# Kernel optimization log

Measured on AMD Instinct MI355X. Metric: run time of the kernel, lower is better.

Reference implementation:

```python
import jax, jax.numpy as jnp
import numpy as np

N_STMT, N_FUNC = 100000, 50000
T, V, C, H, L, E = 16, 50000, 128, 8, 2, 200000
D = C // H  # per-head dim = 16
N_NODES = (N_STMT, N_FUNC)
# (src_type, dst_type) for the 3 relations: stmt->stmt, stmt->func, func->stmt
EDGE_TYPES = ((0, 0), (0, 1), (1, 0))


def _segment_softmax(logits, seg, num_segments):
    # logits: [E, H], seg: [E] destination node ids
    m = jax.ops.segment_max(logits, seg, num_segments)
    m = jnp.where(jnp.isfinite(m), m, 0.0)
    e = jnp.exp(logits - m[seg])
    s = jax.ops.segment_sum(e, seg, num_segments)
    return e / (s[seg] + 1e-16)


def setup_inputs() -> dict:
    key = jax.random.key(0)
    ks = jax.random.split(key, 24)
    nrm = lambda k, sh, s=0.1: jax.random.normal(k, sh, dtype=jnp.float32) * s
    ri = lambda k, sh, hi: jax.random.randint(k, sh, 0, hi, dtype=jnp.int32)
    return {
        "tok_stmt": ri(ks[0], (N_STMT, T), V),
        "tok_func": ri(ks[1], (N_FUNC, T), V),
        "e0_src": ri(ks[2], (E,), N_STMT), "e0_dst": ri(ks[3], (E,), N_STMT),
        "e1_src": ri(ks[4], (E,), N_STMT), "e1_dst": ri(ks[5], (E,), N_FUNC),
        "e2_src": ri(ks[6], (E,), N_FUNC), "e2_dst": ri(ks[7], (E,), N_STMT),
        "emb": nrm(ks[8], (V, C), 0.5),
        "lin_w": nrm(ks[9], (2, C, C)), "lin_b": jnp.zeros((2, C), jnp.float32),
        "kw": nrm(ks[10], (L, 2, C, C)), "kb": jnp.zeros((L, 2, C), jnp.float32),
        "qw": nrm(ks[11], (L, 2, C, C)), "qb": jnp.zeros((L, 2, C), jnp.float32),
        "vw": nrm(ks[12], (L, 2, C, C)), "vb": jnp.zeros((L, 2, C), jnp.float32),
        "aw": nrm(ks[13], (L, 2, C, C)), "ab": jnp.zeros((L, 2, C), jnp.float32),
        "skip": jnp.ones((L, 2), jnp.float32),
        "a_rel": nrm(ks[14], (L, 3, H, D, D), 0.25),
        "m_rel": nrm(ks[15], (L, 3, H, D, D), 0.25),
        "p_rel": jnp.ones((L, 3, H), jnp.float32),
    }


def _hgt_forward(tok_stmt, tok_func, edges, emb, lin_w, lin_b,
                 kw, kb, qw, qb, vw, vb, aw, ab, skip, a_rel, m_rel, p_rel):
    # STEncoder (embedding + mean pool) + relu, then per-type linear + relu
    xs = []
    for t, tok in enumerate((tok_stmt, tok_func)):
        e = jax.nn.relu(jnp.mean(emb[tok], axis=1))          # [N_t, C]
        xs.append(jax.nn.relu(e @ lin_w[t] + lin_b[t]))      # [N_t, C]

    scale = 1.0 / jnp.sqrt(jnp.float32(D))
    for l in range(L):
        k = [(x @ kw[l, t] + kb[l, t]).reshape(-1, H, D) for t, x in enumerate(xs)]
        q = [(x @ qw[l, t] + qb[l, t]).reshape(-1, H, D) for t, x in enumerate(xs)]
        v = [(x @ vw[l, t] + vb[l, t]).reshape(-1, H, D) for t, x in enumerate(xs)]
        agg = [jnp.zeros((N_NODES[t], H, D), xs[t].dtype) for t in range(2)]
        for r, (st, dt) in enumerate(EDGE_TYPES):
            src, dst = edges[r]
            k_r = jnp.einsum('nhd,hde->nhe', k[st], a_rel[l, r])
            v_r = jnp.einsum('nhd,hde->nhe', v[st], m_rel[l, r])
            logits = jnp.sum(q[dt][dst] * k_r[src], axis=-1) * p_rel[l, r] * scale  # [E,H]
            alpha = _segment_softmax(logits, dst, N_NODES[dt])
            msg = v_r[src] * alpha[..., None]                 # [E,H,D]
            agg[dt] = agg[dt] + jax.ops.segment_sum(msg, dst, N_NODES[dt])
        new_xs = []
        for t in range(2):
            o = jax.nn.gelu(agg[t].reshape(N_NODES[t], C))
            o = o @ aw[l, t] + ab[l, t]
            g = jax.nn.sigmoid(skip[l, t])
            new_xs.append(g * o + (1.0 - g) * xs[t])
        xs = new_xs
    return jnp.concatenate(xs, axis=0)  # [N_STMT + N_FUNC, C]


def reference(tok_stmt, tok_func, e0_src, e0_dst, e1_src, e1_dst, e2_src, e2_dst,
              emb, lin_w, lin_b, kw, kb, qw, qb, vw, vb, aw, ab, skip,
              a_rel, m_rel, p_rel):
    edges = ((e0_src, e0_dst), (e1_src, e1_dst), (e2_src, e2_dst))
    return _hgt_forward(tok_stmt, tok_func, edges, emb, lin_w, lin_b,
                        kw, kb, qw, qb, vw, vb, aw, ab, skip, a_rel, m_rel, p_rel)
```

## Files before the change

### kernel.cpp

```cpp
#include <hip/hip_runtime.h>
#include <hip/hip_bf16.h>


typedef __hip_bfloat16 bf16;
typedef __attribute__((ext_vector_type(8))) short short8;
typedef __attribute__((ext_vector_type(4))) short s4v;
typedef __attribute__((ext_vector_type(4))) float floatx4;

#define N_STMT 100000
#define N_FUNC 50000
#define N_TOT  150000
#define EDGES  200000
#define CCH 128
#define RPB2 96
#define GS2 1042
#define GF2 521

__device__ __forceinline__ float b2f(bf16 x){ return __bfloat162float(x); }
__device__ __forceinline__ float bs2f(short s){
  union { short s; bf16 h; } u; u.s = s; return __bfloat162float(u.h);
}
__device__ __forceinline__ short f2bs(float x){
  union { bf16 h; short s; } u; u.h = __float2bfloat16(x); return u.s;
}
__device__ __forceinline__ float blo(unsigned u){ return __uint_as_float(u << 16); }
__device__ __forceinline__ float bhi(unsigned u){ return __uint_as_float(u & 0xffff0000u); }
__device__ __forceinline__ float gelu_f(float x){
  float z = 1.5957691216057308f * (x + 0.044715f * x * x * x);
  float t = __expf(z);
  return x - x / (t + 1.f);
}

__global__ __launch_bounds__(256) void emb2bf(
    const float* __restrict__ emb, bf16* __restrict__ ebf)
{
  long i = ((long)blockIdx.x * 256 + threadIdx.x) * 8;
  float4 f0 = *(const float4*)(emb + i);
  float4 f1 = *(const float4*)(emb + i + 4);
  short8 o;
  o[0]=f2bs(f0.x); o[1]=f2bs(f0.y); o[2]=f2bs(f0.z); o[3]=f2bs(f0.w);
  o[4]=f2bs(f1.x); o[5]=f2bs(f1.y); o[6]=f2bs(f1.z); o[7]=f2bs(f1.w);
  *(short8*)(ebf + i) = o;
}

__global__ __launch_bounds__(256) void pool_embed(
    const int* __restrict__ tok_s, const int* __restrict__ tok_f,
    const bf16* __restrict__ ebf, bf16* __restrict__ E_out)
{
  int n = blockIdx.x * 4 + (threadIdx.x >> 6);
  int lane = threadIdx.x & 63, g = lane >> 4, c16 = lane & 15;
  const int* tok = (n < N_STMT) ? (tok_s + n * 16) : (tok_f + (n - N_STMT) * 16);
  float acc[8] = {0.f,0.f,0.f,0.f,0.f,0.f,0.f,0.f};
#pragma unroll
  for (int j = 0; j < 4; j++) {
    int v = tok[g * 4 + j];
    short8 row = *(const short8*)(ebf + (long)v * CCH + c16 * 8);
#pragma unroll
    for (int q = 0; q < 8; q++) acc[q] += bs2f(row[q]);
  }
#pragma unroll
  for (int q = 0; q < 8; q++) {
    acc[q] += __shfl_xor(acc[q], 16);
    acc[q] += __shfl_xor(acc[q], 32);
  }
  if (g == 0) {
    short8 o;
#pragma unroll
    for (int q = 0; q < 8; q++) o[q] = f2bs(fmaxf(acc[q] * (1.f/16.f), 0.f));
    *(short8*)(E_out + (long)n * CCH + c16 * 8) = o;
  }
}

__global__ __launch_bounds__(256) void transp_w(
    const float* __restrict__ lin_w, const float* __restrict__ qw,
    const float* __restrict__ aw, bf16* __restrict__ out)
{
  int mat = blockIdx.y;
  const float* src = (mat < 2) ? lin_w + mat * 16384
                   : (mat < 6) ? qw + (mat - 2) * 16384
                               : aw + (mat - 6) * 16384;
  bf16* dst = out + mat * 16384;
  int idx = blockIdx.x * 256 + threadIdx.x;
  int n = idx >> 7, k = idx & 127;
  dst[idx] = __float2bfloat16(src[k * 128 + n]);
}

__global__ __launch_bounds__(256) void make_wr_all(
    const float* __restrict__ kw, const float* __restrict__ kb,
    const float* __restrict__ vw, const float* __restrict__ vb,
    const float* __restrict__ a_rel, const float* __restrict__ m_rel,
    bf16* __restrict__ WRT, float* __restrict__ Bf)
{
  int y = blockIdx.y;
  bool isV = y >= 6;
  int z = isV ? y - 6 : y;
  int l = z / 3, r = z % 3, st = (r == 2) ? 1 : 0;
  const float* W   = (isV ? vw : kw) + (l * 2 + st) * 16384;
  const float* b   = (isV ? vb : kb) + (l * 2 + st) * 128;
  const float* rel = (isV ? m_rel : a_rel) + z * 2048;
  bf16* Wrt = WRT + y * 16384;
  float* br = Bf + y * 128;

  int idx = blockIdx.x * 256 + threadIdx.x;
  if (idx < 128 * 128) {
    int c = idx >> 7, o = idx & 127;
    int h = o >> 4, e = o & 15;
    float acc = 0.f;
#pragma unroll
    for (int d = 0; d < 16; d++)
      acc += W[c * 128 + h * 16 + d] * rel[h * 256 + d * 16 + e];
    Wrt[o * 128 + c] = __float2bfloat16(acc);
  }
  if (idx < 128) {
    int h = idx >> 4, e = idx & 15;
    float acc = 0.f;
#pragma unroll
    for (int d = 0; d < 16; d++)
      acc += b[h * 16 + d] * rel[h * 256 + d * 16 + e];
    br[idx] = acc;
  }
}

template <bool RELU, bool BLEND, bool OUT_BF16>
__global__ __launch_bounds__(256) void gemm_2t_reg(
    const bf16* __restrict__ Ab, const bf16* __restrict__ Wt0,
    const bf16* __restrict__ Wt1, const float* __restrict__ bias0,
    const float* __restrict__ bias1, const bf16* __restrict__ oldx,
    void* __restrict__ dstv, const float* __restrict__ skip2)
{
  const int wave = threadIdx.x >> 6, lane = threadIdx.x & 63;
  const int lane15 = lane & 15, quad = lane >> 4;
  const int jc0 = wave * 2;
  const int bid = blockIdx.x;
  const int type = (bid >= GS2);
  const long base = type ? (long)N_STMT * CCH : 0;
  const int Nrows = type ? N_FUNC : N_STMT;
  long row = (long)(type ? bid - GS2 : bid) * RPB2;
  long rowEnd = row + RPB2; if (rowEnd > Nrows) rowEnd = Nrows;
  const bf16* Wt = type ? Wt1 : Wt0;
  const float* bias = type ? bias1 : bias0;

  short8 w[2][4];
#pragma unroll
  for (int jj = 0; jj < 2; jj++)
#pragma unroll
    for (int kq = 0; kq < 4; kq++)
      w[jj][kq] = *(const short8*)(
          Wt + ((jc0 + jj) * 16 + lane15) * CCH + kq * 32 + quad * 8);
  float4 bb[2];
#pragma unroll
  for (int jj = 0; jj < 2; jj++)
    bb[jj] = *(const float4*)(bias + (jc0 + jj) * 16 + quad * 4);

  float g = 1.f, gi = 0.f;
  if (BLEND) {
    float sk = skip2[type];
    g = 1.f / (1.f + expf(-sk));
    gi = 1.f - g;
  }

  short8 a[4];
  {
    long r = row + lane15; if (r >= Nrows) r = Nrows - 1;
#pragma unroll
    for (int kq = 0; kq < 4; kq++)
      a[kq] = *(const short8*)(Ab + base + r * CCH + kq * 32 + quad * 8);
  }

  for (; row < rowEnd; row += 16) {
    short8 an[4];
    {
      long nrow = (row + 16 < rowEnd) ? row + 16 : row;
      long r = nrow + lane15; if (r >= Nrows) r = Nrows - 1;
#pragma unroll
      for (int kq = 0; kq < 4; kq++)
        an[kq] = *(const short8*)(Ab + base + r * CCH + kq * 32 + quad * 8);
    }

    floatx4 acc[2];
#pragma unroll
    for (int jj = 0; jj < 2; jj++) {
      acc[jj][0] = bb[jj].x; acc[jj][1] = bb[jj].y;
      acc[jj][2] = bb[jj].z; acc[jj][3] = bb[jj].w;
    }
#pragma unroll
    for (int kq = 0; kq < 4; kq++)
#pragma unroll
      for (int jj = 0; jj < 2; jj++)
        acc[jj] = __builtin_amdgcn_mfma_f32_16x16x32_bf16(
            w[jj][kq], a[kq], acc[jj], 0, 0, 0);

    long r = row + lane15;
    if (r < Nrows) {
#pragma unroll
      for (int jj = 0; jj < 2; jj++) {
        int c0 = (jc0 + jj) * 16 + quad * 4;
        long idx = base + r * CCH + c0;
        float v[4];
#pragma unroll
        for (int q = 0; q < 4; q++) v[q] = acc[jj][q];
        if (RELU) {
#pragma unroll
          for (int q = 0; q < 4; q++) v[q] = fmaxf(v[q], 0.f);
        }
        if (BLEND) {
          s4v ov = *(const s4v*)(oldx + idx);
#pragma unroll
          for (int q = 0; q < 4; q++) v[q] = g * v[q] + gi * bs2f(ov[q]);
        }
        if (OUT_BF16) {
          s4v o;
#pragma unroll
          for (int q = 0; q < 4; q++) o[q] = f2bs(v[q]);
          *(s4v*)((bf16*)dstv + idx) = o;
        } else {
          float4 o = make_float4(v[0], v[1], v[2], v[3]);
          *(float4*)((float*)dstv + idx) = o;
        }
      }
    }
#pragma unroll
    for (int kq = 0; kq < 4; kq++) a[kq] = an[kq];
  }
}

template <int NM, bool HASQ>
__global__ __launch_bounds__(256, (NM == 2 ? 4 : 3)) void gemm_qkv_reg(
    const bf16* __restrict__ Ab,
    const bf16* __restrict__ W0, const float* __restrict__ B0,
    const bf16* __restrict__ W1, const float* __restrict__ B1,
    const bf16* __restrict__ W2, const float* __restrict__ B2,
    bf16* __restrict__ Q, bf16* __restrict__ KV, int N, int rpb)
{
  const int wave = threadIdx.x >> 6, lane = threadIdx.x & 63;
  const int lane15 = lane & 15, quad = lane >> 4;
  const int jc0 = wave * 2;
  constexpr int KIDX = HASQ ? 1 : 0;
  constexpr int VIDX = KIDX + 1;

  long row = (long)blockIdx.x * rpb;
  if (row >= N) return;
  long rowEnd = row + rpb; if (rowEnd > N) rowEnd = N;

  const bf16* Wm[3]  = {W0, W1, W2};
  const float* Bm[3] = {B0, B1, B2};

  short8 w[NM][2][4];
#pragma unroll
  for (int m = 0; m < NM; m++)
#pragma unroll
    for (int jj = 0; jj < 2; jj++)
#pragma unroll
      for (int kq = 0; kq < 4; kq++)
        w[m][jj][kq] = *(const short8*)(
            Wm[m] + ((jc0 + jj) * 16 + lane15) * CCH + kq * 32 + quad * 8);

  for (; row < rowEnd; row += 16) {
    long r = row + lane15;
    long rc = (r < N) ? r : (N - 1);
    short8 a[4];
#pragma unroll
    for (int kq = 0; kq < 4; kq++)
      a[kq] = *(const short8*)(Ab + rc * CCH + kq * 32 + quad * 8);

    floatx4 acc[NM][2];
#pragma unroll
    for (int m = 0; m < NM; m++)
#pragma unroll
      for (int jj = 0; jj < 2; jj++) {
        float4 bb = *(const float4*)(Bm[m] + (jc0 + jj) * 16 + quad * 4);
        acc[m][jj][0] = bb.x; acc[m][jj][1] = bb.y;
        acc[m][jj][2] = bb.z; acc[m][jj][3] = bb.w;
      }

#pragma unroll
    for (int kq = 0; kq < 4; kq++)
#pragma unroll
      for (int m = 0; m < NM; m++)
#pragma unroll
        for (int jj = 0; jj < 2; jj++)
          acc[m][jj] = __builtin_amdgcn_mfma_f32_16x16x32_bf16(
              w[m][jj][kq], a[kq], acc[m][jj], 0, 0, 0);

    if (r < N) {
#pragma unroll
      for (int jj = 0; jj < 2; jj++) {
        int c0 = (jc0 + jj) * 16 + quad * 4;
        if constexpr (HASQ) {
          s4v qo;
          qo[0] = f2bs(acc[0][jj][0]);
          qo[1] = f2bs(acc[0][jj][1]);
          qo[2] = f2bs(acc[0][jj][2]);
          qo[3] = f2bs(acc[0][jj][3]);
          *(s4v*)(Q + r * CCH + c0) = qo;
        }
        short8 kv;
        kv[0] = f2bs(acc[KIDX][jj][0]);
        kv[1] = f2bs(acc[KIDX][jj][1]);
        kv[2] = f2bs(acc[VIDX][jj][0]);
        kv[3] = f2bs(acc[VIDX][jj][1]);
        kv[4] = f2bs(acc[KIDX][jj][2]);
        kv[5] = f2bs(acc[KIDX][jj][3]);
        kv[6] = f2bs(acc[VIDX][jj][2]);
        kv[7] = f2bs(acc[VIDX][jj][3]);
        *(short8*)(KV + r * 256 + 2 * c0) = kv;
      }
    }
  }
}

__global__ __launch_bounds__(256) void csr_count(
    const int* __restrict__ dst, int* __restrict__ deg, int* __restrict__ pos)
{
  int e = blockIdx.x * 256 + threadIdx.x;
  if (e < EDGES) pos[e] = atomicAdd(&deg[dst[e]], 1);
}
__global__ __launch_bounds__(256) void csr_alloc(
    const int* __restrict__ deg, int* __restrict__ rowstart,
    int* __restrict__ total, int Ndst)
{
  int n = blockIdx.x * 256 + threadIdx.x;
  if (n < Ndst) rowstart[n] = atomicAdd(total, deg[n]);
}
__global__ __launch_bounds__(256) void csr_fill(
    const int* __restrict__ dst, const int* __restrict__ src,
    const int* __restrict__ rowstart, const int* __restrict__ pos,
    int* __restrict__ srcs)
{
  int e = blockIdx.x * 256 + threadIdx.x;
  if (e < EDGES) srcs[rowstart[dst[e]] + pos[e]] = src[e];
}

__device__ __forceinline__ void relmsg_grp(
    int rs, int g, const int* __restrict__ srcs,
    const bf16* __restrict__ KV, float psc,
    const float* __restrict__ q, int lane, float* __restrict__ out)
{
  int p = lane & 15;
  int gbase = lane & 48;
  float den = 0.f;
  float a[8] = {0.f,0.f,0.f,0.f,0.f,0.f,0.f,0.f};
  for (int j0 = 0; j0 < g; j0 += 16) {
    int rem = g - j0; if (rem > 16) rem = 16;
    int sl = srcs[rs + j0 + (p < rem ? p : rem - 1)];
    for (int j = 0; j < rem; j++) {
      int s = __shfl(sl, gbase + j);
      const bf16* rowp = KV + (long)s * 256 + 16 * p;
      uint4 u0 = *(const uint4*)(rowp);
      uint4 u1 = *(const uint4*)(rowp + 8);
      float prod = q[0]*blo(u0.x) + q[1]*bhi(u0.x)
                 + q[2]*blo(u0.z) + q[3]*bhi(u0.z)
                 + q[4]*blo(u1.x) + q[5]*bhi(u1.x)
                 + q[6]*blo(u1.z) + q[7]*bhi(u1.z);
      prod += __shfl_xor(prod, 1);
      float ev = __expf(prod * psc);
      den += ev;
      a[0] += ev * blo(u0.y); a[1] += ev * bhi(u0.y);
      a[2] += ev * blo(u0.w); a[3] += ev * bhi(u0.w);
      a[4] += ev * blo(u1.y); a[5] += ev * bhi(u1.y);
      a[6] += ev * blo(u1.w); a[7] += ev * bhi(u1.w);
    }
  }
  float inv = 1.f / (den + 1e-16f);
#pragma unroll
  for (int i = 0; i < 8; i++) out[i] = a[i] * inv;
}

__global__ __launch_bounds__(256) void agg_all(
    const int* __restrict__ rs0, const int* __restrict__ dg0, const int* __restrict__ srcs0,
    const int* __restrict__ rs1, const int* __restrict__ dg1, const int* __restrict__ srcs1,
    const int* __restrict__ rs2, const int* __restrict__ dg2, const int* __restrict__ srcs2,
    const bf16* __restrict__ KV0, const bf16* __restrict__ KV1,
    const bf16* __restrict__ KV2, const float* __restrict__ pl,
    const bf16* __restrict__ Qb, bf16* __restrict__ AGGb)
{
  int n = blockIdx.x * 16 + (threadIdx.x >> 4);
  if (n >= N_TOT) return;
  int lane = threadIdx.x & 63;
  int p = lane & 15, h = p >> 1;
  uint4 qv = *(const uint4*)(Qb + (long)n * CCH + 8 * p);
  float q[8];
  q[0] = blo(qv.x); q[1] = bhi(qv.x); q[2] = blo(qv.y); q[3] = bhi(qv.y);
  q[4] = blo(qv.z); q[5] = bhi(qv.z); q[6] = blo(qv.w); q[7] = bhi(qv.w);
  float m[8];
  if (n < N_STMT) {
    float m0[8], m2[8];
    relmsg_grp(rs0[n], dg0[n], srcs0, KV0, pl[h] * 0.25f, q, lane, m0);
    relmsg_grp(rs2[n], dg2[n], srcs2, KV2, pl[16 + h] * 0.25f, q, lane, m2);
#pragma unroll
    for (int i = 0; i < 8; i++) m[i] = m0[i] + m2[i];
  } else {
    int nf = n - N_STMT;
    relmsg_grp(rs1[nf], dg1[nf], srcs1, KV1, pl[8 + h] * 0.25f, q, lane, m);
  }
  short8 o;
#pragma unroll
  for (int i = 0; i < 8; i++) o[i] = f2bs(gelu_f(m[i]));
  *(short8*)(AGGb + (long)n * CCH + 8 * p) = o;
}

__global__ __launch_bounds__(256) void zero_out_k(float* __restrict__ out)
{
  long i = ((long)blockIdx.x * 256 + threadIdx.x) * 4;
  *(float4*)(out + i) = make_float4(0.f, 0.f, 0.f, 0.f);
}

extern "C" void kernel_launch(void* const* d_in, const int* in_sizes, int n_in,
                              void* d_out, int out_size, void* d_ws, size_t ws_size,
                              hipStream_t stream)
{
  const int* tok_s = (const int*)d_in[0];
  const int* tok_f = (const int*)d_in[1];
  const int* esrc[3] = {(const int*)d_in[2], (const int*)d_in[4], (const int*)d_in[6]};
  const int* edst[3] = {(const int*)d_in[3], (const int*)d_in[5], (const int*)d_in[7]};
  const float* emb   = (const float*)d_in[8];
  const float* lin_w = (const float*)d_in[9];
  const float* lin_b = (const float*)d_in[10];
  const float* kw = (const float*)d_in[11];
  const float* kb = (const float*)d_in[12];
  const float* qw = (const float*)d_in[13];
  const float* qb = (const float*)d_in[14];
  const float* vw = (const float*)d_in[15];
  const float* vb = (const float*)d_in[16];
  const float* aw = (const float*)d_in[17];
  const float* ab = (const float*)d_in[18];
  const float* skip  = (const float*)d_in[19];
  const float* a_rel = (const float*)d_in[20];
  const float* m_rel = (const float*)d_in[21];
  const float* p_rel = (const float*)d_in[22];

  float* Bf   = (float*)d_ws;
  bf16*  Xb   = (bf16*)(Bf + 1536);
  bf16*  AGGb = Xb  + 19200000L;
  bf16*  KV0  = AGGb + 19200000L;
  bf16*  KV1  = KV0 + 25600000L;
  bf16*  KV2  = KV1 + 25600000L;
  bf16*  WT   = KV2 + 12800000L;
  bf16*  WRT  = WT  + 163840L;
  int*   ip   = (int*)(WRT + 196608L);
  int* deg[3]      = {ip, ip + 100000, ip + 150000};
  int* total       = ip + 250000;
  int* rowstart[3] = {ip + 250004, ip + 350004, ip + 400004};
  int* srcs[3]     = {ip + 500004, ip + 700004, ip + 900004};
  int* pos         = ip + 1100004;
  bf16* EBF   = KV0;
  bf16*  Qb   = (bf16*)d_out;
  float* OUTF = (float*)d_out;

  const size_t NEED = (size_t)1536 * 4 + (size_t)102760448 * 2
                    + (size_t)1300004 * 4;
  if (ws_size < NEED) {
    zero_out_k<<<19200000 / 4 / 256, 256, 0, stream>>>(OUTF);
    return;
  }

  const int  Ntype[2] = {N_STMT, N_FUNC};
  const int  edt[3] = {0, 1, 0};
  const int  EB = (EDGES + 255) / 256;

  hipMemsetAsync(ip, 0, (size_t)250004 * 4, stream);
  for (int r = 0; r < 3; r++) {
    int Nd = Ntype[edt[r]];
    csr_count<<<EB, 256, 0, stream>>>(edst[r], deg[r], pos);
    csr_alloc<<<(Nd + 255) / 256, 256, 0, stream>>>(deg[r], rowstart[r], total + r, Nd);
    csr_fill<<<EB, 256, 0, stream>>>(edst[r], esrc[r], rowstart[r], pos, srcs[r]);
  }

  emb2bf<<<3125, 256, 0, stream>>>(emb, EBF);
  transp_w<<<dim3(64, 10), 256, 0, stream>>>(lin_w, qw, aw, WT);
  make_wr_all<<<dim3(64, 12), 256, 0, stream>>>(kw, kb, vw, vb, a_rel, m_rel, WRT, Bf);

  pool_embed<<<N_TOT / 4, 256, 0, stream>>>(tok_s, tok_f, EBF, AGGb);
  gemm_2t_reg<true, false, true><<<GS2 + GF2, 256, 0, stream>>>(
      AGGb, WT, WT + 16384, lin_b, lin_b + 128, nullptr, Xb, nullptr);

  const int GA = (N_STMT + 127) / 128;
  const int GB = (N_STMT + 95) / 96;
  const int GF = (N_FUNC + 127) / 128;

  for (int l = 0; l < 2; l++) {
    int z0 = l * 3 + 0, z1 = l * 3 + 1, z2 = l * 3 + 2;
    gemm_qkv_reg<3, true><<<GA, 256, 0, stream>>>(
        Xb,
        WT + (2 + l * 2) * 16384, qb + (l * 2) * 128,
        WRT + z0 * 16384, Bf + z0 * 128,
        WRT + (6 + z0) * 16384, Bf + (6 + z0) * 128,
        Qb, KV0, N_STMT, 128);
    gemm_qkv_reg<2, false><<<GB, 256, 0, stream>>>(
        Xb,
        WRT + z1 * 16384, Bf + z1 * 128,
        WRT + (6 + z1) * 16384, Bf + (6 + z1) * 128,
        nullptr, nullptr,
        nullptr, KV1, N_STMT, 96);
    gemm_qkv_reg<3, true><<<GF, 256, 0, stream>>>(
        Xb + (long)N_STMT * CCH,
        WT + (2 + l * 2 + 1) * 16384, qb + (l * 2 + 1) * 128,
        WRT + z2 * 16384, Bf + z2 * 128,
        WRT + (6 + z2) * 16384, Bf + (6 + z2) * 128,
        Qb + (long)N_STMT * CCH, KV2, N_FUNC, 128);
    agg_all<<<(N_TOT + 15) / 16, 256, 0, stream>>>(
        rowstart[0], deg[0], srcs[0], rowstart[1], deg[1], srcs[1],
        rowstart[2], deg[2], srcs[2], KV0, KV1, KV2,
        p_rel + l * 24, Qb, AGGb);
    if (l == 0)
      gemm_2t_reg<false, true, true><<<GS2 + GF2, 256, 0, stream>>>(
          AGGb, WT + 6 * 16384, WT + 7 * 16384, ab, ab + 128,
          Xb, Xb, skip);
    else
      gemm_2t_reg<false, true, false><<<GS2 + GF2, 256, 0, stream>>>(
          AGGb, WT + 8 * 16384, WT + 9 * 16384, ab + 256, ab + 384,
          Xb, OUTF, skip + 2);
  }
}
```

Before: 719.5 us.

## Fuse embedding mean-pool with per-type input linear layer via MFMA

Replaces the separate pooling kernel and the following GEMM with a single kernel. Each block pools 64 rows into LDS as bf16 A-fragments and immediately applies the per-type 128x128 linear, bias and ReLU with MFMA. This removes the write and re-read of the intermediate pooled matrix and one launch. In exchange, weights are reloaded per 64-row block and each thread holds more gather accumulators, which may lower occupancy.

```diff
diff --git a/kernel.cpp b/kernel.cpp
--- a/kernel.cpp
+++ b/kernel.cpp
@@ -15,6 +15,8 @@
 #define RPB2 96
 #define GS2 1042
 #define GF2 521
+#define GSP 1563
+#define GFP 782
 
 __device__ __forceinline__ float b2f(bf16 x){ return __bfloat162float(x); }
 __device__ __forceinline__ float bs2f(short s){
@@ -43,31 +45,103 @@
   *(short8*)(ebf + i) = o;
 }
 
-__global__ __launch_bounds__(256) void pool_embed(
+__global__ __launch_bounds__(256, 3) void pool_lin(
     const int* __restrict__ tok_s, const int* __restrict__ tok_f,
-    const bf16* __restrict__ ebf, bf16* __restrict__ E_out)
-{
-  int n = blockIdx.x * 4 + (threadIdx.x >> 6);
-  int lane = threadIdx.x & 63, g = lane >> 4, c16 = lane & 15;
-  const int* tok = (n < N_STMT) ? (tok_s + n * 16) : (tok_f + (n - N_STMT) * 16);
-  float acc[8] = {0.f,0.f,0.f,0.f,0.f,0.f,0.f,0.f};
-#pragma unroll
-  for (int j = 0; j < 4; j++) {
-    int v = tok[g * 4 + j];
-    short8 row = *(const short8*)(ebf + (long)v * CCH + c16 * 8);
-#pragma unroll
-    for (int q = 0; q < 8; q++) acc[q] += bs2f(row[q]);
-  }
-#pragma unroll
-  for (int q = 0; q < 8; q++) {
-    acc[q] += __shfl_xor(acc[q], 16);
-    acc[q] += __shfl_xor(acc[q], 32);
-  }
-  if (g == 0) {
+    const bf16* __restrict__ ebf,
+    const bf16* __restrict__ Wt0, const bf16* __restrict__ Wt1,
+    const float* __restrict__ bias0, const float* __restrict__ bias1,
+    bf16* __restrict__ Xb)
+{
+  __shared__ short8 Afrag[4][64][4];
+  const int wave = threadIdx.x >> 6, lane = threadIdx.x & 63;
+  const int lane15 = lane & 15, quad = lane >> 4;
+  const int bid = blockIdx.x;
+  const int type = (bid >= GSP);
+  const long rbase = type ? (long)N_STMT : 0;
+  const int Nrows = type ? N_FUNC : N_STMT;
+  const long brow = (long)(type ? bid - GSP : bid) * 64;
+  const int* tokp = type ? tok_f : tok_s;
+  const bf16* Wt = type ? Wt1 : Wt0;
+  const float* bias = type ? bias1 : bias0;
+
+  long prow = brow + wave * 16 + lane15;
+  long prc = (prow < Nrows) ? prow : (Nrows - 1);
+  const int* trow = tokp + prc * 16;
+  int tt0 = trow[quad * 4 + 0], tt1 = trow[quad * 4 + 1];
+  int tt2 = trow[quad * 4 + 2], tt3 = trow[quad * 4 + 3];
+
+  float acc[4][8];
+#pragma unroll
+  for (int kq = 0; kq < 4; kq++)
+#pragma unroll
+    for (int i = 0; i < 8; i++) acc[kq][i] = 0.f;
+
+#pragma unroll
+  for (int t = 0; t < 16; t++) {
+    int reg = t & 3;
+    int v = __shfl(reg == 0 ? tt0 : reg == 1 ? tt1 : reg == 2 ? tt2 : tt3,
+                   (t >> 2) * 16 + lane15);
+    const bf16* rp = ebf + (long)v * CCH + quad * 8;
+#pragma unroll
+    for (int kq = 0; kq < 4; kq++) {
+      short8 u = *(const short8*)(rp + kq * 32);
+#pragma unroll
+      for (int i = 0; i < 8; i++) acc[kq][i] += bs2f(u[i]);
+    }
+  }
+#pragma unroll
+  for (int kq = 0; kq < 4; kq++) {
     short8 o;
 #pragma unroll
-    for (int q = 0; q < 8; q++) o[q] = f2bs(fmaxf(acc[q] * (1.f/16.f), 0.f));
-    *(short8*)(E_out + (long)n * CCH + c16 * 8) = o;
+    for (int i = 0; i < 8; i++)
+      o[i] = f2bs(fmaxf(acc[kq][i] * (1.f / 16.f), 0.f));
+    Afrag[wave][lane][kq] = o;
+  }
+  __syncthreads();
+
+  const int jc0 = wave * 2;
+  short8 w[2][4];
+#pragma unroll
+  for (int jj = 0; jj < 2; jj++)
+#pragma unroll
+    for (int kq = 0; kq < 4; kq++)
+      w[jj][kq] = *(const short8*)(
+          Wt + ((jc0 + jj) * 16 + lane15) * CCH + kq * 32 + quad * 8);
+  float4 bb[2];
+#pragma unroll
+  for (int jj = 0; jj < 2; jj++)
+    bb[jj] = *(const float4*)(bias + (jc0 + jj) * 16 + quad * 4);
+
+#pragma unroll
+  for (int tt = 0; tt < 4; tt++) {
+    short8 a[4];
+#pragma unroll
+    for (int kq = 0; kq < 4; kq++) a[kq] = Afrag[tt][lane][kq];
+
+    floatx4 ac[2];
+#pragma unroll
+    for (int jj = 0; jj < 2; jj++) {
+      ac[jj][0] = bb[jj].x; ac[jj][1] = bb[jj].y;
+      ac[jj][2] = bb[jj].z; ac[jj][3] = bb[jj].w;
+    }
+#pragma unroll
+    for (int kq = 0; kq < 4; kq++)
+#pragma unroll
+      for (int jj = 0; jj < 2; jj++)
+        ac[jj] = __builtin_amdgcn_mfma_f32_16x16x32_bf16(
+            w[jj][kq], a[kq], ac[jj], 0, 0, 0);
+
+    long r = brow + tt * 16 + lane15;
+    if (r < Nrows) {
+#pragma unroll
+      for (int jj = 0; jj < 2; jj++) {
+        int c0 = (jc0 + jj) * 16 + quad * 4;
+        s4v o;
+#pragma unroll
+        for (int q = 0; q < 4; q++) o[q] = f2bs(fmaxf(ac[jj][q], 0.f));
+        *(s4v*)(Xb + (rbase + r) * CCH + c0) = o;
+      }
+    }
   }
 }
 
@@ -470,9 +544,8 @@
   transp_w<<<dim3(64, 10), 256, 0, stream>>>(lin_w, qw, aw, WT);
   make_wr_all<<<dim3(64, 12), 256, 0, stream>>>(kw, kb, vw, vb, a_rel, m_rel, WRT, Bf);
 
-  pool_embed<<<N_TOT / 4, 256, 0, stream>>>(tok_s, tok_f, EBF, AGGb);
-  gemm_2t_reg<true, false, true><<<GS2 + GF2, 256, 0, stream>>>(
-      AGGb, WT, WT + 16384, lin_b, lin_b + 128, nullptr, Xb, nullptr);
+  pool_lin<<<GSP + GFP, 256, 0, stream>>>(
+      tok_s, tok_f, EBF, WT, WT + 16384, lin_b, lin_b + 128, Xb);
 
   const int GA = (N_STMT + 127) / 128;
   const int GB = (N_STMT + 95) / 96;
```

Result: no change. 720.9 us (+0.2%).
